# Optimization experiments

Measured on AMD Instinct MI355X. Metric: run time of the kernel, lower is better.

The kernel has to match this reference:

```python
import jax, jax.numpy as jnp
import numpy as np

# ---- static forest structure: 1024 complete binary trees of depth 9 ----
N_TREES = 1024
DEPTH = 9
NPT = 2 ** (DEPTH + 1) - 1            # 1023 nodes per tree
DIM = N_TREES * NPT                    # 1,047,552 total nodes
C = 10                                 # hidden states
M = 128                                # emission alphabet
N_GEN = 4                              # parallel generative models
LEVEL_SIZES = [N_TREES * 2 ** (k + 1) for k in range(DEPTH)]
LEVEL_START = np.concatenate([[0], np.cumsum(LEVEL_SIZES)]).astype(np.int64)
TREE_OFF = np.arange(N_TREES, dtype=np.int64) * NPT


def _build_forest():
    parents, children = [], []
    for k in range(DEPTH):
        ch = np.arange(2 ** (k + 1) - 1, 2 ** (k + 2) - 1, dtype=np.int64)  # depth k+1 nodes
        pa = (ch - 1) // 2                                                   # their parents (depth k)
        children.append((TREE_OFF[:, None] + ch[None, :]).ravel())
        parents.append((TREE_OFF[:, None] + pa[None, :]).ravel())
    leaves = (TREE_OFF[:, None] + np.arange(NPT // 2, NPT, dtype=np.int64)[None, :]).ravel()
    trees_ind = np.repeat(np.arange(N_TREES, dtype=np.int64), NPT)
    return np.concatenate(parents), np.concatenate(children), leaves, trees_ind


def setup_inputs() -> dict:
    key = jax.random.key(0)
    k1, k2, k3, k4 = jax.random.split(key, 4)
    parents, children, leaves, trees_ind = _build_forest()
    return {
        "x": jax.random.randint(k4, (DIM,), 0, M, dtype=jnp.int32),
        "A": jax.random.normal(k1, (C, C, N_GEN), jnp.float32) * 2.5,
        "B": jax.random.normal(k2, (C, M, N_GEN), jnp.float32) * 2.5,
        "Pi": jax.random.normal(k3, (C, N_GEN), jnp.float32) * 2.5,
        "parents": jnp.asarray(parents, jnp.int32),
        "children": jnp.asarray(children, jnp.int32),
        "trees_ind": jnp.asarray(trees_ind, jnp.int32),
        "leaves": jnp.asarray(leaves, jnp.int32),
    }


def _upward(x, A, B, Pi, parents, children, trees_ind, leaves):
    # softmax reparameterization (vectorized over the n_gen axis)
    smA = jax.nn.softmax(A, axis=0)    # P(parent state i | child state j), cols sum over i
    smB = jax.nn.softmax(B, axis=1)    # emission distribution per state
    smPi = jax.nn.softmax(Pi, axis=0)  # leaf prior

    beta = jnp.zeros((DIM, C, N_GEN), smA.dtype)
    t_beta = jnp.zeros((DIM, C, N_GEN), smA.dtype)
    ll = jnp.zeros((DIM, N_GEN), smA.dtype)

    # leaves: beta = Pi * B[:, x_leaf], normalized
    B_leaf = jnp.swapaxes(smB[:, x[leaves]], 0, 1)            # [L, C, G]
    b = smPi[None, :, :] * B_leaf
    nu = b.sum(axis=1)                                         # [L, G]
    beta = beta.at[leaves].set(b / nu[:, None, :])
    ll = ll.at[leaves].set(jnp.log(nu))

    # bottom-up sweep over levels (static loop over tree depth)
    for k in reversed(range(DEPTH)):
        s, e = int(LEVEL_START[k]), int(LEVEL_START[k + 1])
        pa, ch = parents[s:e], children[s:e]
        beta_ch = beta[ch]                                     # [E, C, G]
        tb_ch = jnp.einsum('ijg,ejg->eig', smA, beta_ch)       # sum over child state j
        sums = jax.ops.segment_sum(tb_ch, pa, num_segments=DIM)
        cnt = jax.ops.segment_sum(jnp.ones((e - s,), smA.dtype), pa, num_segments=DIM)
        t_beta = t_beta + sums / jnp.maximum(cnt, 1.0)[:, None, None]  # scatter-mean over children
        # unique parents at this level = all depth-k nodes (static for complete trees)
        u = jnp.asarray((TREE_OFF[:, None] + np.arange(2 ** k - 1, 2 ** (k + 1) - 1)[None, :]).ravel(), jnp.int32)
        B_u = jnp.swapaxes(smB[:, x[u]], 0, 1)                 # [U, C, G]
        bl = t_beta[u] * B_u
        nu = bl.sum(axis=1)
        beta = beta.at[u].set(bl / nu[:, None, :])
        ll = ll.at[u].set(jnp.log(nu))

    # per-tree log-likelihood: scatter-sum node terms over trees_ind
    return jax.ops.segment_sum(ll, trees_ind, num_segments=N_TREES)  # [n_trees, G]


def reference(x, A, B, Pi, parents, children, trees_ind, leaves):
    return _upward(x, A, B, Pi, parents, children, trees_ind, leaves)
```

## Files before the change

kernel.cpp:

```cpp
#include <hip/hip_runtime.h>
#include <math.h>

#define NC     10
#define NCP    12
#define NM     128
#define NGEN   4
#define NPT    1023
#define NTREES 1024

#define RCPF(x) __builtin_amdgcn_rcpf(x)
#define WAVE_FENCE() __builtin_amdgcn_wave_barrier()

struct F12 { float4 a, b, c; };

__device__ __forceinline__ F12 ld12(const float* p) {
    F12 r; const float4* q = (const float4*)p;
    r.a = q[0]; r.b = q[1]; r.c = q[2]; return r;
}
__device__ __forceinline__ void unpack10(float* t, const F12& r) {
    t[0] = r.a.x; t[1] = r.a.y; t[2] = r.a.z; t[3] = r.a.w;
    t[4] = r.b.x; t[5] = r.b.y; t[6] = r.b.z; t[7] = r.b.w;
    t[8] = r.c.x; t[9] = r.c.y;
}
__device__ __forceinline__ void fma10(float* t, const F12& c, float s) {
    t[0] += c.a.x * s; t[1] += c.a.y * s; t[2] += c.a.z * s; t[3] += c.a.w * s;
    t[4] += c.b.x * s; t[5] += c.b.y * s; t[6] += c.b.z * s; t[7] += c.b.w * s;
    t[8] += c.c.x * s; t[9] += c.c.y * s;
}
__device__ __forceinline__ void mul10(float* t, const F12& r) {
    t[0] *= r.a.x; t[1] *= r.a.y; t[2] *= r.a.z; t[3] *= r.a.w;
    t[4] *= r.b.x; t[5] *= r.b.y; t[6] *= r.b.z; t[7] *= r.b.w;
    t[8] *= r.c.x; t[9] *= r.c.y;
}
__device__ __forceinline__ float sum10(const float* v) {
    return (((v[0] + v[1]) + (v[2] + v[3])) + ((v[4] + v[5]) + (v[6] + v[7]))) + (v[8] + v[9]);
}

__device__ __forceinline__ float group3_leaf(const F12* acol, const float (*bt)[NCP],
                                             const float (*btpi)[NCP],
                                             int xl0, int xl1, int xp, float* bout) {
    float b0[NC], b1[NC];
    unpack10(b0, ld12(&btpi[xl0][0]));
    unpack10(b1, ld12(&btpi[xl1][0]));
    const float nu0 = sum10(b0), nu1 = sum10(b1);
    float t[NC];
    #pragma unroll
    for (int i = 0; i < NC; ++i) t[i] = 0.f;
    #pragma unroll
    for (int j = 0; j < NC; ++j) fma10(t, acol[j], b0[j] * nu1 + b1[j] * nu0);
    mul10(t, ld12(&bt[xp][0]));
    const float nup = sum10(t);
    const float r = RCPF(nup);
    #pragma unroll
    for (int j = 0; j < NC; ++j) bout[j] = t[j] * r;
    return __logf(nup);
}

__device__ __forceinline__ float node_unnorm(const F12* acol, const float (*bt)[NCP],
                                             const float* c0, const float* c1,
                                             int xv, float* uo) {
    float t[NC];
    #pragma unroll
    for (int i = 0; i < NC; ++i) t[i] = 0.f;
    #pragma unroll
    for (int j = 0; j < NC; ++j) fma10(t, acol[j], c0[j] + c1[j]);
    mul10(t, ld12(&bt[xv][0]));
    #pragma unroll
    for (int j = 0; j < NC; ++j) uo[j] = t[j];
    return sum10(t);
}

__device__ __forceinline__ float group3_mid(const F12* acol, const float (*bt)[NCP],
                                            const float* u0, float nu0,
                                            const float* u1, float nu1,
                                            int xp, float* bout) {
    float t[NC];
    #pragma unroll
    for (int i = 0; i < NC; ++i) t[i] = 0.f;
    #pragma unroll
    for (int j = 0; j < NC; ++j) fma10(t, acol[j], u0[j] * nu1 + u1[j] * nu0);
    mul10(t, ld12(&bt[xp][0]));
    const float nup = sum10(t);
    const float r = RCPF(nup);
    #pragma unroll
    for (int j = 0; j < NC; ++j) bout[j] = t[j] * r;
    return __logf(nup);
}

__device__ __forceinline__ float fused_step_ip(const F12* acol, const float (*bt)[NCP],
                                               float* buf, int l,
                                               int xc0, int xc1, int xp)
{
    float t0[NC], t1[NC];
    #pragma unroll
    for (int i = 0; i < NC; ++i) { t0[i] = 0.f; t1[i] = 0.f; }
    #pragma unroll
    for (int j = 0; j < NC; ++j) {
        float4 gv = *(const float4*)(buf + j * 64 + 4 * l);
        fma10(t0, acol[j], gv.x + gv.y);
        fma10(t1, acol[j], gv.z + gv.w);
    }
    mul10(t0, ld12(&bt[xc0][0]));
    mul10(t1, ld12(&bt[xc1][0]));
    const float nu0 = sum10(t0), nu1 = sum10(t1);
    float tp[NC];
    #pragma unroll
    for (int i = 0; i < NC; ++i) tp[i] = 0.f;
    #pragma unroll
    for (int j = 0; j < NC; ++j) fma10(tp, acol[j], t0[j] * nu1 + t1[j] * nu0);
    mul10(tp, ld12(&bt[xp][0]));
    const float nup = sum10(tp);
    const float rp = RCPF(nup);
    #pragma unroll
    for (int j = 0; j < NC; ++j) buf[j * 64 + l] = tp[j] * rp;
    return __logf(nup);
}

__global__ __launch_bounds__(256)
void htmm_fused(const int* __restrict__ x,
                const float* __restrict__ A,
                const float* __restrict__ B,
                const float* __restrict__ Pi,
                float* __restrict__ out)
{
    __shared__ __align__(16) float sACol[NC][NCP];
    __shared__ __align__(16) float sBT[NM][NCP];
    __shared__ __align__(16) float sBTpi[NM][NCP];
    __shared__ __align__(16) float sPiP[NCP];
    __shared__ __align__(16) float sB6[4][NC][64];

    const int bid = blockIdx.x;
    const int g = bid >> 8;
    const int treeBase = (bid & 255) * 4;
    const int tid = threadIdx.x;
    const int u = tid >> 6, lane = tid & 63;

    const int tree = treeBase + u;
    const int tb = tree * NPT;

    int xl[8];
    #pragma unroll
    for (int k = 0; k < 8; ++k) xl[k] = x[tb + 511 + 8 * lane + k];
    int x8v[4];
    #pragma unroll
    for (int c = 0; c < 4; ++c) x8v[c] = x[tb + 255 + 4 * lane + c];
    const int x7a = x[tb + 127 + 2 * lane];
    const int x7b = x[tb + 128 + 2 * lane];
    const int x6v = x[tb + 63 + lane];

    for (int c = u; c < NC; c += 4) {
        float e0 = __expf(B[(c * NM + lane) * NGEN + g]);
        float e1 = __expf(B[(c * NM + lane + 64) * NGEN + g]);
        float sm = e0 + e1;
        #pragma unroll
        for (int off = 32; off; off >>= 1) sm += __shfl_xor(sm, off);
        const float rs = 1.f / sm;
        sBT[lane][c]      = e0 * rs;
        sBT[lane + 64][c] = e1 * rs;
    }
    if (tid >= 128 && tid < 128 + NC) {
        const int j = tid - 128;
        float col[NC], mx = -1e30f;
        #pragma unroll
        for (int i = 0; i < NC; ++i) { col[i] = A[(i * NC + j) * NGEN + g]; mx = fmaxf(mx, col[i]); }
        float sm = 0.f;
        #pragma unroll
        for (int i = 0; i < NC; ++i) { col[i] = __expf(col[i] - mx); sm += col[i]; }
        const float rs = 0.5f / sm;
        #pragma unroll
        for (int i = 0; i < NC; ++i) sACol[j][i] = col[i] * rs;
    }
    if (tid == 192) {
        float col[NC], mx = -1e30f;
        #pragma unroll
        for (int i = 0; i < NC; ++i) { col[i] = Pi[i * NGEN + g]; mx = fmaxf(mx, col[i]); }
        float sm = 0.f;
        #pragma unroll
        for (int i = 0; i < NC; ++i) { col[i] = __expf(col[i] - mx); sm += col[i]; }
        const float rs = 1.f / sm;
        #pragma unroll
        for (int i = 0; i < NC; ++i) sPiP[i] = col[i] * rs;
    }
    __syncthreads();
    if (tid < NM) {
        F12 pi = ld12(sPiP);
        F12 r  = ld12(&sBT[tid][0]);
        sBTpi[tid][0] = pi.a.x * r.a.x; sBTpi[tid][1] = pi.a.y * r.a.y;
        sBTpi[tid][2] = pi.a.z * r.a.z; sBTpi[tid][3] = pi.a.w * r.a.w;
        sBTpi[tid][4] = pi.b.x * r.b.x; sBTpi[tid][5] = pi.b.y * r.b.y;
        sBTpi[tid][6] = pi.b.z * r.b.z; sBTpi[tid][7] = pi.b.w * r.b.w;
        sBTpi[tid][8] = pi.c.x * r.c.x; sBTpi[tid][9] = pi.c.y * r.c.y;
    }
    __syncthreads();

    F12 acol[NC];
    #pragma unroll
    for (int j = 0; j < NC; ++j) acol[j] = ld12(&sACol[j][0]);

    float llacc;
    float ba[NC], bb[NC], u7a[NC], u7b[NC];

    llacc  = group3_leaf(acol, sBT, sBTpi, xl[0], xl[1], x8v[0], ba);
    llacc += group3_leaf(acol, sBT, sBTpi, xl[2], xl[3], x8v[1], bb);
    const float nu7a = node_unnorm(acol, sBT, ba, bb, x7a, u7a);

    llacc += group3_leaf(acol, sBT, sBTpi, xl[4], xl[5], x8v[2], ba);
    llacc += group3_leaf(acol, sBT, sBTpi, xl[6], xl[7], x8v[3], bb);
    const float nu7b = node_unnorm(acol, sBT, ba, bb, x7b, u7b);

    llacc += group3_mid(acol, sBT, u7a, nu7a, u7b, nu7b, x6v, ba);
    #pragma unroll
    for (int j = 0; j < NC; ++j) sB6[u][j][lane] = ba[j];

    WAVE_FENCE();
    float lla = 0.f;
    if (lane < 16)
        lla = fused_step_ip(acol, sBT, &sB6[u][0][0], lane,
                            x[tb + 31 + 2 * lane], x[tb + 32 + 2 * lane],
                            x[tb + 15 + lane]);
    llacc += lla;
    WAVE_FENCE();
    float llb = 0.f;
    if (lane < 4)
        llb = fused_step_ip(acol, sBT, &sB6[u][0][0], lane,
                            x[tb + 7 + 2 * lane], x[tb + 8 + 2 * lane],
                            x[tb + 3 + lane]);
    llacc += llb;
    WAVE_FENCE();
    if (lane == 0)
        llacc += fused_step_ip(acol, sBT, &sB6[u][0][0], 0,
                               x[tb + 1], x[tb + 2], x[tb + 0]);

    #pragma unroll
    for (int off = 32; off; off >>= 1) llacc += __shfl_down(llacc, off);
    if (lane == 0) out[tree * NGEN + g] = llacc;
}

extern "C" void kernel_launch(void* const* d_in, const int* in_sizes, int n_in,
                              void* d_out, int out_size, void* d_ws, size_t ws_size,
                              hipStream_t stream) {
    const int*   x  = (const int*)d_in[0];
    const float* A  = (const float*)d_in[1];
    const float* B  = (const float*)d_in[2];
    const float* Pi = (const float*)d_in[3];
    float* out = (float*)d_out;
    htmm_fused<<<NTREES, 256, 0, stream>>>(x, A, B, Pi, out);
}
```

Before: 26.06 us.

## Split softmax setup into prologue kernel and store emission table as bf16

Adds a small setup kernel that computes the softmaxed A, Pi and a bf16-packed transposed emission table once per generative model into workspace. The main kernel then only copies that 4 KB table into LDS instead of redoing exps and reductions in each of the 1024 blocks, and it multiplies by Pi on the fly. It also keeps the old fused kernel inline as a fallback when the workspace is too small. The trade-offs are an extra kernel launch plus a dependency, and reduced precision in the emission probabilities from bf16 rounding.

```diff
diff --git a/kernel.cpp b/kernel.cpp
--- a/kernel.cpp
+++ b/kernel.cpp
@@ -2,12 +2,17 @@
 #include <math.h>
 
 #define NC     10
-#define NCP    12
+#define ACP    12
 #define NM     128
 #define NGEN   4
 #define NPT    1023
 #define NTREES 1024
 
+#define WS_AC(g)   ((g) * (NC * ACP))
+#define WS_PI(g)   (4 * NC * ACP + (g) * ACP)
+#define WS_BT(g)   (4 * NC * ACP + 4 * ACP + (g) * (NM * 8))
+#define WS_FLOATS  (4 * NC * ACP + 4 * ACP + 4 * NM * 8)
+
 #define RCPF(x) __builtin_amdgcn_rcpf(x)
 #define WAVE_FENCE() __builtin_amdgcn_wave_barrier()
 
@@ -27,28 +32,39 @@
     t[4] += c.b.x * s; t[5] += c.b.y * s; t[6] += c.b.z * s; t[7] += c.b.w * s;
     t[8] += c.c.x * s; t[9] += c.c.y * s;
 }
-__device__ __forceinline__ void mul10(float* t, const F12& r) {
-    t[0] *= r.a.x; t[1] *= r.a.y; t[2] *= r.a.z; t[3] *= r.a.w;
-    t[4] *= r.b.x; t[5] *= r.b.y; t[6] *= r.b.z; t[7] *= r.b.w;
-    t[8] *= r.c.x; t[9] *= r.c.y;
-}
 __device__ __forceinline__ float sum10(const float* v) {
     return (((v[0] + v[1]) + (v[2] + v[3])) + ((v[4] + v[5]) + (v[6] + v[7]))) + (v[8] + v[9]);
 }
 
-__device__ __forceinline__ float group3_leaf(const F12* acol, const float (*bt)[NCP],
-                                             const float (*btpi)[NCP],
+__device__ __forceinline__ void ldrow10(const unsigned int* t16, int m, float* o) {
+    const unsigned int* p = t16 + m * 8;
+    uint4 d = *(const uint4*)p;
+    unsigned int q = p[4];
+    o[0] = __uint_as_float(d.x << 16); o[1] = __uint_as_float(d.x & 0xffff0000u);
+    o[2] = __uint_as_float(d.y << 16); o[3] = __uint_as_float(d.y & 0xffff0000u);
+    o[4] = __uint_as_float(d.z << 16); o[5] = __uint_as_float(d.z & 0xffff0000u);
+    o[6] = __uint_as_float(d.w << 16); o[7] = __uint_as_float(d.w & 0xffff0000u);
+    o[8] = __uint_as_float(q << 16);   o[9] = __uint_as_float(q & 0xffff0000u);
+}
+
+__device__ __forceinline__ float group3_leaf(const F12* acol, const unsigned int* bt16,
+                                             const float* piv,
                                              int xl0, int xl1, int xp, float* bout) {
+    float r0[NC], r1[NC], rp[NC];
+    ldrow10(bt16, xl0, r0);
+    ldrow10(bt16, xl1, r1);
+    ldrow10(bt16, xp, rp);
     float b0[NC], b1[NC];
-    unpack10(b0, ld12(&btpi[xl0][0]));
-    unpack10(b1, ld12(&btpi[xl1][0]));
+    #pragma unroll
+    for (int j = 0; j < NC; ++j) { b0[j] = piv[j] * r0[j]; b1[j] = piv[j] * r1[j]; }
     const float nu0 = sum10(b0), nu1 = sum10(b1);
     float t[NC];
     #pragma unroll
     for (int i = 0; i < NC; ++i) t[i] = 0.f;
     #pragma unroll
     for (int j = 0; j < NC; ++j) fma10(t, acol[j], b0[j] * nu1 + b1[j] * nu0);
-    mul10(t, ld12(&bt[xp][0]));
+    #pragma unroll
+    for (int i = 0; i < NC; ++i) t[i] *= rp[i];
     const float nup = sum10(t);
     const float r = RCPF(nup);
     #pragma unroll
@@ -56,30 +72,34 @@
     return __logf(nup);
 }
 
-__device__ __forceinline__ float node_unnorm(const F12* acol, const float (*bt)[NCP],
+__device__ __forceinline__ float node_unnorm(const F12* acol, const unsigned int* bt16,
                                              const float* c0, const float* c1,
                                              int xv, float* uo) {
+    float rp[NC];
+    ldrow10(bt16, xv, rp);
     float t[NC];
     #pragma unroll
     for (int i = 0; i < NC; ++i) t[i] = 0.f;
     #pragma unroll
     for (int j = 0; j < NC; ++j) fma10(t, acol[j], c0[j] + c1[j]);
-    mul10(t, ld12(&bt[xv][0]));
-    #pragma unroll
-    for (int j = 0; j < NC; ++j) uo[j] = t[j];
+    #pragma unroll
+    for (int i = 0; i < NC; ++i) { t[i] *= rp[i]; uo[i] = t[i]; }
     return sum10(t);
 }
 
-__device__ __forceinline__ float group3_mid(const F12* acol, const float (*bt)[NCP],
+__device__ __forceinline__ float group3_mid(const F12* acol, const unsigned int* bt16,
                                             const float* u0, float nu0,
                                             const float* u1, float nu1,
                                             int xp, float* bout) {
+    float rp[NC];
+    ldrow10(bt16, xp, rp);
     float t[NC];
     #pragma unroll
     for (int i = 0; i < NC; ++i) t[i] = 0.f;
     #pragma unroll
     for (int j = 0; j < NC; ++j) fma10(t, acol[j], u0[j] * nu1 + u1[j] * nu0);
-    mul10(t, ld12(&bt[xp][0]));
+    #pragma unroll
+    for (int i = 0; i < NC; ++i) t[i] *= rp[i];
     const float nup = sum10(t);
     const float r = RCPF(nup);
     #pragma unroll
@@ -87,10 +107,14 @@
     return __logf(nup);
 }
 
-__device__ __forceinline__ float fused_step_ip(const F12* acol, const float (*bt)[NCP],
+__device__ __forceinline__ float fused_step_ip(const F12* acol, const unsigned int* bt16,
                                                float* buf, int l,
                                                int xc0, int xc1, int xp)
 {
+    float rc0[NC], rc1[NC], rp[NC];
+    ldrow10(bt16, xc0, rc0);
+    ldrow10(bt16, xc1, rc1);
+    ldrow10(bt16, xp, rp);
     float t0[NC], t1[NC];
     #pragma unroll
     for (int i = 0; i < NC; ++i) { t0[i] = 0.f; t1[i] = 0.f; }
@@ -100,22 +124,178 @@
         fma10(t0, acol[j], gv.x + gv.y);
         fma10(t1, acol[j], gv.z + gv.w);
     }
-    mul10(t0, ld12(&bt[xc0][0]));
-    mul10(t1, ld12(&bt[xc1][0]));
+    #pragma unroll
+    for (int i = 0; i < NC; ++i) { t0[i] *= rc0[i]; t1[i] *= rc1[i]; }
     const float nu0 = sum10(t0), nu1 = sum10(t1);
     float tp[NC];
     #pragma unroll
     for (int i = 0; i < NC; ++i) tp[i] = 0.f;
     #pragma unroll
     for (int j = 0; j < NC; ++j) fma10(tp, acol[j], t0[j] * nu1 + t1[j] * nu0);
-    mul10(tp, ld12(&bt[xp][0]));
+    #pragma unroll
+    for (int i = 0; i < NC; ++i) tp[i] *= rp[i];
     const float nup = sum10(tp);
-    const float rp = RCPF(nup);
-    #pragma unroll
-    for (int j = 0; j < NC; ++j) buf[j * 64 + l] = tp[j] * rp;
+    const float rpn = RCPF(nup);
+    #pragma unroll
+    for (int j = 0; j < NC; ++j) buf[j * 64 + l] = tp[j] * rpn;
     return __logf(nup);
 }
 
+__global__ __launch_bounds__(128)
+void htmm_setup(const float* __restrict__ A,
+                const float* __restrict__ B,
+                const float* __restrict__ Pi,
+                float* __restrict__ ws)
+{
+    __shared__ float sm[NC][NM];
+    const int g = blockIdx.x;
+    const int tid = threadIdx.x;
+    const int wave = tid >> 6, lane = tid & 63;
+
+    for (int c = wave; c < NC; c += 2) {
+        float e0 = __expf(B[(c * NM + lane) * NGEN + g]);
+        float e1 = __expf(B[(c * NM + lane + 64) * NGEN + g]);
+        float s = e0 + e1;
+        #pragma unroll
+        for (int off = 32; off; off >>= 1) s += __shfl_xor(s, off);
+        const float rs = 1.f / s;
+        sm[c][lane] = e0 * rs;
+        sm[c][lane + 64] = e1 * rs;
+    }
+    if (tid < NC) {
+        const int j = tid;
+        float col[NC], mx = -1e30f;
+        #pragma unroll
+        for (int i = 0; i < NC; ++i) { col[i] = A[(i * NC + j) * NGEN + g]; mx = fmaxf(mx, col[i]); }
+        float s = 0.f;
+        #pragma unroll
+        for (int i = 0; i < NC; ++i) { col[i] = __expf(col[i] - mx); s += col[i]; }
+        const float rs = 0.5f / s;
+        float* ac = ws + WS_AC(g) + j * ACP;
+        #pragma unroll
+        for (int i = 0; i < NC; ++i) ac[i] = col[i] * rs;
+        ac[10] = 0.f; ac[11] = 0.f;
+    }
+    if (tid == 16) {
+        float col[NC], mx = -1e30f;
+        #pragma unroll
+        for (int i = 0; i < NC; ++i) { col[i] = Pi[i * NGEN + g]; mx = fmaxf(mx, col[i]); }
+        float s = 0.f;
+        #pragma unroll
+        for (int i = 0; i < NC; ++i) { col[i] = __expf(col[i] - mx); s += col[i]; }
+        const float rs = 1.f / s;
+        float* pp = ws + WS_PI(g);
+        #pragma unroll
+        for (int i = 0; i < NC; ++i) pp[i] = col[i] * rs;
+        pp[10] = 0.f; pp[11] = 0.f;
+    }
+    __syncthreads();
+
+    {
+        const int m = tid;
+        unsigned int* bt = (unsigned int*)(ws + WS_BT(g)) + m * 8;
+        unsigned int d[5];
+        #pragma unroll
+        for (int k = 0; k < 5; ++k) {
+            unsigned int u0 = __float_as_uint(sm[2 * k][m]);
+            unsigned int u1 = __float_as_uint(sm[2 * k + 1][m]);
+            unsigned int b0 = (u0 + 0x7fffu + ((u0 >> 16) & 1u)) >> 16;
+            unsigned int b1 = (u1 + 0x7fffu + ((u1 >> 16) & 1u)) >> 16;
+            d[k] = b0 | (b1 << 16);
+        }
+        bt[0] = d[0]; bt[1] = d[1]; bt[2] = d[2]; bt[3] = d[3]; bt[4] = d[4];
+        bt[5] = 0u; bt[6] = 0u; bt[7] = 0u;
+    }
+}
+
+__global__ __launch_bounds__(256)
+void htmm_main(const int* __restrict__ x,
+               const float* __restrict__ ws,
+               float* __restrict__ out)
+{
+    __shared__ __align__(16) unsigned int sBT16[NM * 8];
+    __shared__ __align__(16) float sB6[4][NC][64];
+
+    const int bid = blockIdx.x;
+    const int g = bid >> 8;
+    const int treeBase = (bid & 255) * 4;
+    const int tid = threadIdx.x;
+    const int u = tid >> 6, lane = tid & 63;
+
+    const int tree = treeBase + u;
+    const int tb = tree * NPT;
+
+    {
+        const unsigned int* src = (const unsigned int*)(ws + WS_BT(g));
+        uint4 v = *(const uint4*)(src + tid * 4);
+        *(uint4*)(sBT16 + tid * 4) = v;
+    }
+
+    int xl[8];
+    #pragma unroll
+    for (int k = 0; k < 8; ++k) xl[k] = x[tb + 511 + 8 * lane + k];
+    int x8v[4];
+    #pragma unroll
+    for (int c = 0; c < 4; ++c) x8v[c] = x[tb + 255 + 4 * lane + c];
+    const int x7a = x[tb + 127 + 2 * lane];
+    const int x7b = x[tb + 128 + 2 * lane];
+    const int x6v = x[tb + 63 + lane];
+
+    F12 acol[NC];
+    #pragma unroll
+    for (int j = 0; j < NC; ++j) acol[j] = ld12(ws + WS_AC(g) + j * ACP);
+    float piv[NC];
+    {
+        F12 pv = ld12(ws + WS_PI(g));
+        unpack10(piv, pv);
+    }
+    __syncthreads();
+
+    float llacc;
+    float ba[NC], bb[NC], u7a[NC], u7b[NC];
+
+    llacc  = group3_leaf(acol, sBT16, piv, xl[0], xl[1], x8v[0], ba);
+    llacc += group3_leaf(acol, sBT16, piv, xl[2], xl[3], x8v[1], bb);
+    const float nu7a = node_unnorm(acol, sBT16, ba, bb, x7a, u7a);
+
+    llacc += group3_leaf(acol, sBT16, piv, xl[4], xl[5], x8v[2], ba);
+    llacc += group3_leaf(acol, sBT16, piv, xl[6], xl[7], x8v[3], bb);
+    const float nu7b = node_unnorm(acol, sBT16, ba, bb, x7b, u7b);
+
+    llacc += group3_mid(acol, sBT16, u7a, nu7a, u7b, nu7b, x6v, ba);
+    #pragma unroll
+    for (int j = 0; j < NC; ++j) sB6[u][j][lane] = ba[j];
+
+    WAVE_FENCE();
+    float lla = 0.f;
+    if (lane < 16)
+        lla = fused_step_ip(acol, sBT16, &sB6[u][0][0], lane,
+                            x[tb + 31 + 2 * lane], x[tb + 32 + 2 * lane],
+                            x[tb + 15 + lane]);
+    llacc += lla;
+    WAVE_FENCE();
+    float llb = 0.f;
+    if (lane < 4)
+        llb = fused_step_ip(acol, sBT16, &sB6[u][0][0], lane,
+                            x[tb + 7 + 2 * lane], x[tb + 8 + 2 * lane],
+                            x[tb + 3 + lane]);
+    llacc += llb;
+    WAVE_FENCE();
+    if (lane == 0)
+        llacc += fused_step_ip(acol, sBT16, &sB6[u][0][0], 0,
+                               x[tb + 1], x[tb + 2], x[tb + 0]);
+
+    #pragma unroll
+    for (int off = 32; off; off >>= 1) llacc += __shfl_down(llacc, off);
+    if (lane == 0) out[tree * NGEN + g] = llacc;
+}
+
+__device__ __forceinline__ void mul10f(float* t, const F12& r) {
+    t[0] *= r.a.x; t[1] *= r.a.y; t[2] *= r.a.z; t[3] *= r.a.w;
+    t[4] *= r.b.x; t[5] *= r.b.y; t[6] *= r.b.z; t[7] *= r.b.w;
+    t[8] *= r.c.x; t[9] *= r.c.y;
+}
+#define NCP 12
 __global__ __launch_bounds__(256)
 void htmm_fused(const int* __restrict__ x,
                 const float* __restrict__ A,
@@ -134,7 +314,6 @@
     const int treeBase = (bid & 255) * 4;
     const int tid = threadIdx.x;
     const int u = tid >> 6, lane = tid & 63;
-
     const int tree = treeBase + u;
     const int tb = tree * NPT;
 
@@ -200,36 +379,157 @@
     float llacc;
     float ba[NC], bb[NC], u7a[NC], u7b[NC];
 
-    llacc  = group3_leaf(acol, sBT, sBTpi, xl[0], xl[1], x8v[0], ba);
-    llacc += group3_leaf(acol, sBT, sBTpi, xl[2], xl[3], x8v[1], bb);
-    const float nu7a = node_unnorm(acol, sBT, ba, bb, x7a, u7a);
-
-    llacc += group3_leaf(acol, sBT, sBTpi, xl[4], xl[5], x8v[2], ba);
-    llacc += group3_leaf(acol, sBT, sBTpi, xl[6], xl[7], x8v[3], bb);
-    const float nu7b = node_unnorm(acol, sBT, ba, bb, x7b, u7b);
-
-    llacc += group3_mid(acol, sBT, u7a, nu7a, u7b, nu7b, x6v, ba);
-    #pragma unroll
-    for (int j = 0; j < NC; ++j) sB6[u][j][lane] = ba[j];
+    {
+        float b0[NC], b1[NC], t[NC];
+        unpack10(b0, ld12(&sBTpi[xl[0]][0])); unpack10(b1, ld12(&sBTpi[xl[1]][0]));
+        float nu0 = sum10(b0), nu1 = sum10(b1);
+        #pragma unroll
+        for (int i = 0; i < NC; ++i) t[i] = 0.f;
+        #pragma unroll
+        for (int j = 0; j < NC; ++j) fma10(t, acol[j], b0[j] * nu1 + b1[j] * nu0);
+        mul10f(t, ld12(&sBT[x8v[0]][0]));
+        float nup = sum10(t); float r = RCPF(nup);
+        #pragma unroll
+        for (int j = 0; j < NC; ++j) ba[j] = t[j] * r;
+        llacc = __logf(nup);
+        unpack10(b0, ld12(&sBTpi[xl[2]][0])); unpack10(b1, ld12(&sBTpi[xl[3]][0]));
+        nu0 = sum10(b0); nu1 = sum10(b1);
+        #pragma unroll
+        for (int i = 0; i < NC; ++i) t[i] = 0.f;
+        #pragma unroll
+        for (int j = 0; j < NC; ++j) fma10(t, acol[j], b0[j] * nu1 + b1[j] * nu0);
+        mul10f(t, ld12(&sBT[x8v[1]][0]));
+        nup = sum10(t); r = RCPF(nup);
+        #pragma unroll
+        for (int j = 0; j < NC; ++j) bb[j] = t[j] * r;
+        llacc += __logf(nup);
+        #pragma unroll
+        for (int i = 0; i < NC; ++i) t[i] = 0.f;
+        #pragma unroll
+        for (int j = 0; j < NC; ++j) fma10(t, acol[j], ba[j] + bb[j]);
+        mul10f(t, ld12(&sBT[x7a][0]));
+        #pragma unroll
+        for (int i = 0; i < NC; ++i) u7a[i] = t[i];
+        const float nu7a = sum10(t);
+        unpack10(b0, ld12(&sBTpi[xl[4]][0])); unpack10(b1, ld12(&sBTpi[xl[5]][0]));
+        nu0 = sum10(b0); nu1 = sum10(b1);
+        #pragma unroll
+        for (int i = 0; i < NC; ++i) t[i] = 0.f;
+        #pragma unroll
+        for (int j = 0; j < NC; ++j) fma10(t, acol[j], b0[j] * nu1 + b1[j] * nu0);
+        mul10f(t, ld12(&sBT[x8v[2]][0]));
+        nup = sum10(t); r = RCPF(nup);
+        #pragma unroll
+        for (int j = 0; j < NC; ++j) ba[j] = t[j] * r;
+        llacc += __logf(nup);
+        unpack10(b0, ld12(&sBTpi[xl[6]][0])); unpack10(b1, ld12(&sBTpi[xl[7]][0]));
+        nu0 = sum10(b0); nu1 = sum10(b1);
+        #pragma unroll
+        for (int i = 0; i < NC; ++i) t[i] = 0.f;
+        #pragma unroll
+        for (int j = 0; j < NC; ++j) fma10(t, acol[j], b0[j] * nu1 + b1[j] * nu0);
+        mul10f(t, ld12(&sBT[x8v[3]][0]));
+        nup = sum10(t); r = RCPF(nup);
+        #pragma unroll
+        for (int j = 0; j < NC; ++j) bb[j] = t[j] * r;
+        llacc += __logf(nup);
+        #pragma unroll
+        for (int i = 0; i < NC; ++i) t[i] = 0.f;
+        #pragma unroll
+        for (int j = 0; j < NC; ++j) fma10(t, acol[j], ba[j] + bb[j]);
+        mul10f(t, ld12(&sBT[x7b][0]));
+        #pragma unroll
+        for (int i = 0; i < NC; ++i) u7b[i] = t[i];
+        const float nu7b = sum10(t);
+        #pragma unroll
+        for (int i = 0; i < NC; ++i) t[i] = 0.f;
+        #pragma unroll
+        for (int j = 0; j < NC; ++j) fma10(t, acol[j], u7a[j] * nu7b + u7b[j] * nu7a);
+        mul10f(t, ld12(&sBT[x6v][0]));
+        nup = sum10(t); r = RCPF(nup);
+        #pragma unroll
+        for (int j = 0; j < NC; ++j) sB6[u][j][lane] = t[j] * r;
+        llacc += __logf(nup);
+    }
 
     WAVE_FENCE();
-    float lla = 0.f;
-    if (lane < 16)
-        lla = fused_step_ip(acol, sBT, &sB6[u][0][0], lane,
-                            x[tb + 31 + 2 * lane], x[tb + 32 + 2 * lane],
-                            x[tb + 15 + lane]);
-    llacc += lla;
-    WAVE_FENCE();
-    float llb = 0.f;
-    if (lane < 4)
-        llb = fused_step_ip(acol, sBT, &sB6[u][0][0], lane,
-                            x[tb + 7 + 2 * lane], x[tb + 8 + 2 * lane],
-                            x[tb + 3 + lane]);
-    llacc += llb;
-    WAVE_FENCE();
-    if (lane == 0)
-        llacc += fused_step_ip(acol, sBT, &sB6[u][0][0], 0,
-                               x[tb + 1], x[tb + 2], x[tb + 0]);
+    {
+        float lla = 0.f;
+        if (lane < 16) {
+            float t0[NC], t1[NC], tp[NC];
+            #pragma unroll
+            for (int i = 0; i < NC; ++i) { t0[i] = 0.f; t1[i] = 0.f; }
+            float* buf = &sB6[u][0][0];
+            #pragma unroll
+            for (int j = 0; j < NC; ++j) {
+                float4 gv = *(const float4*)(buf + j * 64 + 4 * lane);
+                fma10(t0, acol[j], gv.x + gv.y);
+                fma10(t1, acol[j], gv.z + gv.w);
+            }
+            mul10f(t0, ld12(&sBT[x[tb + 31 + 2 * lane]][0]));
+            mul10f(t1, ld12(&sBT[x[tb + 32 + 2 * lane]][0]));
+            const float nu0 = sum10(t0), nu1 = sum10(t1);
+            #pragma unroll
+            for (int i = 0; i < NC; ++i) tp[i] = 0.f;
+            #pragma unroll
+            for (int j = 0; j < NC; ++j) fma10(tp, acol[j], t0[j] * nu1 + t1[j] * nu0);
+            mul10f(tp, ld12(&sBT[x[tb + 15 + lane]][0]));
+            const float nup = sum10(tp); const float rp = RCPF(nup);
+            #pragma unroll
+            for (int j = 0; j < NC; ++j) buf[j * 64 + lane] = tp[j] * rp;
+            lla = __logf(nup);
+        }
+        llacc += lla;
+        WAVE_FENCE();
+        float llb = 0.f;
+        if (lane < 4) {
+            float t0[NC], t1[NC], tp[NC];
+            #pragma unroll
+            for (int i = 0; i < NC; ++i) { t0[i] = 0.f; t1[i] = 0.f; }
+            float* buf = &sB6[u][0][0];
+            #pragma unroll
+            for (int j = 0; j < NC; ++j) {
+                float4 gv = *(const float4*)(buf + j * 64 + 4 * lane);
+                fma10(t0, acol[j], gv.x + gv.y);
+                fma10(t1, acol[j], gv.z + gv.w);
+            }
+            mul10f(t0, ld12(&sBT[x[tb + 7 + 2 * lane]][0]));
+            mul10f(t1, ld12(&sBT[x[tb + 8 + 2 * lane]][0]));
+            const float nu0 = sum10(t0), nu1 = sum10(t1);
+            #pragma unroll
+            for (int i = 0; i < NC; ++i) tp[i] = 0.f;
+            #pragma unroll
+            for (int j = 0; j < NC; ++j) fma10(tp, acol[j], t0[j] * nu1 + t1[j] * nu0);
+            mul10f(tp, ld12(&sBT[x[tb + 3 + lane]][0]));
+            const float nup = sum10(tp); const float rp = RCPF(nup);
+            #pragma unroll
+            for (int j = 0; j < NC; ++j) buf[j * 64 + lane] = tp[j] * rp;
+            llb = __logf(nup);
+        }
+        llacc += llb;
+        WAVE_FENCE();
+        if (lane == 0) {
+            float t0[NC], t1[NC], tp[NC];
+            #pragma unroll
+            for (int i = 0; i < NC; ++i) { t0[i] = 0.f; t1[i] = 0.f; }
+            float* buf = &sB6[u][0][0];
+            #pragma unroll
+            for (int j = 0; j < NC; ++j) {
+                float4 gv = *(const float4*)(buf + j * 64);
+                fma10(t0, acol[j], gv.x + gv.y);
+                fma10(t1, acol[j], gv.z + gv.w);
+            }
+            mul10f(t0, ld12(&sBT[x[tb + 1]][0]));
+            mul10f(t1, ld12(&sBT[x[tb + 2]][0]));
+            const float nu0 = sum10(t0), nu1 = sum10(t1);
+            #pragma unroll
+            for (int i = 0; i < NC; ++i) tp[i] = 0.f;
+            #pragma unroll
+            for (int j = 0; j < NC; ++j) fma10(tp, acol[j], t0[j] * nu1 + t1[j] * nu0);
+            mul10f(tp, ld12(&sBT[x[tb]][0]));
+            llacc += __logf(sum10(tp));
+        }
+    }
 
     #pragma unroll
     for (int off = 32; off; off >>= 1) llacc += __shfl_down(llacc, off);
@@ -244,5 +544,12 @@
     const float* B  = (const float*)d_in[2];
     const float* Pi = (const float*)d_in[3];
     float* out = (float*)d_out;
-    htmm_fused<<<NTREES, 256, 0, stream>>>(x, A, B, Pi, out);
-}
+
+    if (ws_size >= (size_t)WS_FLOATS * sizeof(float)) {
+        float* ws = (float*)d_ws;
+        htmm_setup<<<NGEN, 128, 0, stream>>>(A, B, Pi, ws);
+        htmm_main<<<NTREES, 256, 0, stream>>>(x, ws, out);
+    } else {
+        htmm_fused<<<NTREES, 256, 0, stream>>>(x, A, B, Pi, out);
+    }
+}
```

Result: slower. 35.04 us (+34.4%).
